# Performance work log

Hardware: AMD Instinct MI355X
Metric: run time of the kernel (lower is better)

## Reference

```python
import jax, jax.numpy as jnp
import numpy as np


def reverse_padded(tokens, lengths):
    # reverse each row within its valid length; padding stays in place
    B, T = tokens.shape
    t = jnp.arange(T)[None, :]
    L = lengths[:, None]
    idx = jnp.where(t < L, L - 1 - t, t)
    return jnp.take_along_axis(tokens, idx, axis=1)


def lstm_layer(x, lengths, Wih, Whh, bih, bhh):
    # x: [T, B, I]; emulates packed LSTM: padded steps output zeros, state frozen
    T, B, _ = x.shape
    H = Whh.shape[1]
    xW = jnp.einsum('tbi,gi->tbg', x, Wih) + bih  # precompute input GEMM [T,B,4H]
    mask = (jnp.arange(T)[:, None] < lengths[None, :]).astype(x.dtype)[:, :, None]

    def step(carry, inp):
        h, c = carry
        xw, m = inp
        gates = xw + h @ Whh.T + bhh
        i, f, g, o = jnp.split(gates, 4, axis=-1)
        i = jax.nn.sigmoid(i); f = jax.nn.sigmoid(f)
        g = jnp.tanh(g); o = jax.nn.sigmoid(o)
        c_new = f * c + i * g
        h_new = o * jnp.tanh(c_new)
        h = m * h_new + (1.0 - m) * h
        c = m * c_new + (1.0 - m) * c
        return (h, c), m * h_new

    h0 = jnp.zeros((B, H), x.dtype)
    (hT, cT), out = jax.lax.scan(step, (h0, h0), (xW, mask))
    return out


def setup_inputs() -> dict:
    key = jax.random.key(0)
    ntoken, ninp, nhid, B, T = 50000, 512, 1024, 64, 512
    ks = jax.random.split(key, 40)
    inp = {}
    inp['input'] = jax.random.randint(ks[0], (B, T), 0, ntoken)
    lens = jnp.sort(jax.random.randint(ks[1], (B,), T // 4, T + 1))[::-1]
    inp['seq_lengths'] = lens.at[0].set(T)
    inp['enc'] = jax.random.uniform(ks[2], (ntoken, ninp), jnp.float32, -0.1, 0.1)
    k = 3
    for d in ('f', 'r'):
        for l in range(2):
            I = ninp if l == 0 else nhid
            s = 1.0 / np.sqrt(nhid)
            inp[f'Wih_{d}{l}'] = jax.random.uniform(ks[k], (4 * nhid, I), jnp.float32, -s, s); k += 1
            inp[f'Whh_{d}{l}'] = jax.random.uniform(ks[k], (4 * nhid, nhid), jnp.float32, -s, s); k += 1
            inp[f'bih_{d}{l}'] = jax.random.uniform(ks[k], (4 * nhid,), jnp.float32, -s, s); k += 1
            inp[f'bhh_{d}{l}'] = jax.random.uniform(ks[k], (4 * nhid,), jnp.float32, -s, s); k += 1
    return inp


def reference(input, seq_lengths, enc,
              Wih_f0, Whh_f0, bih_f0, bhh_f0,
              Wih_f1, Whh_f1, bih_f1, bhh_f1,
              Wih_r0, Whh_r0, bih_r0, bhh_r0,
              Wih_r1, Whh_r1, bih_r1, bhh_r1):
    # eval-mode Elmo forward (all dropouts identity)
    input_rev = reverse_padded(input, seq_lengths)
    emb = enc[input].transpose(1, 0, 2)          # [T,B,ninp]
    emb_rev = enc[input_rev].transpose(1, 0, 2)  # [T,B,ninp]
    h_f = lstm_layer(emb, seq_lengths, Wih_f0, Whh_f0, bih_f0, bhh_f0)
    h_f = lstm_layer(h_f, seq_lengths, Wih_f1, Whh_f1, bih_f1, bhh_f1)
    h_r = lstm_layer(emb_rev, seq_lengths, Wih_r0, Whh_r0, bih_r0, bhh_r0)
    h_r = lstm_layer(h_r, seq_lengths, Wih_r1, Whh_r1, bih_r1, bhh_r1)
    return jnp.concatenate([h_f, h_r], axis=-1)  # [T,B,2*nhid]
```

## Files before the change

### kernel.cpp

```cpp
#include <hip/hip_runtime.h>

#define TT 512
#define BB 64
#define NI 512
#define NH 1024
#define NG 4096

using bf16x8 = __attribute__((ext_vector_type(8))) __bf16;
using f32x4  = __attribute__((ext_vector_type(4))) float;

static __device__ __forceinline__ unsigned short f2bf(float f) {
  unsigned int u = __float_as_uint(f);
  u += 0x7fffu + ((u >> 16) & 1u);
  return (unsigned short)(u >> 16);
}

__global__ void prep_layer(const float* __restrict__ Wih, const float* __restrict__ Whh,
                           const float* __restrict__ bih, const float* __restrict__ bhh,
                           unsigned short* __restrict__ Wx, unsigned short* __restrict__ Wh,
                           float* __restrict__ bias, int Kx) {
  long nx = (long)NG * Kx;
  long nh = (long)NG * NH;
  long total = nx + nh + NG;
  for (long i = (long)blockIdx.x * blockDim.x + threadIdx.x; i < total;
       i += (long)gridDim.x * blockDim.x) {
    if (i < nx) {
      int p = (int)(i / Kx); int k = (int)(i - (long)p * Kx);
      int orig = (p & 3) * NH + (p >> 2);
      Wx[i] = f2bf(Wih[(long)orig * Kx + k]);
    } else if (i < nx + nh) {
      long j = i - nx;
      int p = (int)(j / NH); int k = (int)(j - (long)p * NH);
      int orig = (p & 3) * NH + (p >> 2);
      Wh[j] = f2bf(Whh[(long)orig * NH + k]);
    } else {
      int p = (int)(i - nx - nh);
      int orig = (p & 3) * NH + (p >> 2);
      bias[p] = bih[orig] + bhh[orig];
    }
  }
}

__global__ void prep_emb(const int* __restrict__ tok, const int* __restrict__ lens,
                         const float* __restrict__ enc,
                         unsigned short* __restrict__ embf, unsigned short* __restrict__ embr) {
  int row = blockIdx.x;
  int t = row / BB, b = row - (row / BB) * BB;
  int L = lens[b];
  int tf = tok[b * TT + t];
  int ir = (t < L) ? (L - 1 - t) : t;
  int tr_ = tok[b * TT + ir];
  int i = threadIdx.x;
  float4 vf = *(const float4*)(enc + (long)tf * NI + i * 4);
  float4 vr = *(const float4*)(enc + (long)tr_ * NI + i * 4);
  ushort4 of = make_ushort4(f2bf(vf.x), f2bf(vf.y), f2bf(vf.z), f2bf(vf.w));
  ushort4 orr = make_ushort4(f2bf(vr.x), f2bf(vr.y), f2bf(vr.z), f2bf(vr.w));
  *(ushort4*)(embf + (long)row * NI + i * 4) = of;
  *(ushort4*)(embr + (long)row * NI + i * 4) = orr;
}

struct KP {
  const int* lens;
  const unsigned short* emb[2];
  const unsigned short* Wx[4];
  const unsigned short* Wh[4];
  const float* bias[4];
  unsigned short* hist[4];
  unsigned int* slots;
  float* out;
};

static __device__ __forceinline__ void poll16(const unsigned int* slots, int base,
                                              unsigned tgt) {
  const unsigned int* p = slots + (size_t)(base + ((threadIdx.x & 63) & 15)) * 8;
  for (;;) {
    unsigned v = __hip_atomic_load(p, __ATOMIC_RELAXED, __HIP_MEMORY_SCOPE_AGENT);
    if (__all((int)(v >= tgt))) break;
  }
  asm volatile("" ::: "memory");
}

template <int KQ>
static __device__ __forceinline__ void loadw_q(bf16x8* w, const unsigned short* Wsrc,
                                               int row0, int kbase, int Kfull,
                                               int ln, int kg) {
#pragma unroll
  for (int mt = 0; mt < 4; ++mt) {
    const unsigned short* p = Wsrc + (long)(row0 + mt * 16 + ln) * Kfull + kbase + kg * 8;
#pragma unroll
    for (int ks = 0; ks < KQ; ++ks) w[mt * KQ + ks] = *(const bf16x8*)(p + ks * 32);
  }
}

template <int KQ>
static __device__ __forceinline__ void gemm_row(const bf16x8* w, f32x4* acc,
                                                const unsigned short* src, int stride,
                                                int kbase, int ln, int kg) {
  const unsigned short* p0 = src + (long)ln * stride + kbase + kg * 8;
  const long rs = (long)stride * 16;
  bf16x8 b[KQ][4];
#pragma unroll
  for (int g = 0; g < KQ; ++g)
#pragma unroll
    for (int nt = 0; nt < 4; ++nt) b[g][nt] = *(const bf16x8*)(p0 + nt * rs + g * 32);
  __builtin_amdgcn_s_setprio(1);
#pragma unroll
  for (int ks = 0; ks < KQ; ++ks)
#pragma unroll
    for (int mt = 0; mt < 4; ++mt)
#pragma unroll
      for (int nt = 0; nt < 4; ++nt)
        acc[mt * 4 + nt] = __builtin_amdgcn_mfma_f32_16x16x32_bf16(
            w[mt * KQ + ks], b[ks][nt], acc[mt * 4 + nt], 0, 0, 0);
  __builtin_amdgcn_s_setprio(0);
}

template <int KQ>
static __device__ __forceinline__ void gemm_blk(const bf16x8* w, f32x4* acc,
                                                const unsigned short* src, int kbase,
                                                int ln, int kg) {
  const unsigned short* p0 = src + ((kbase >> 4) + (kg >> 1)) * 1024 + ln * 16 + (kg & 1) * 8;
  bf16x8 b[4][4];
#pragma unroll
  for (int g = 0; g < 4; ++g)
#pragma unroll
    for (int nt = 0; nt < 4; ++nt) b[g][nt] = *(const bf16x8*)(p0 + nt * 256 + g * 2048);
#pragma unroll
  for (int ks = 0; ks < KQ; ++ks) {
    __builtin_amdgcn_s_setprio(1);
#pragma unroll
    for (int mt = 0; mt < 4; ++mt)
#pragma unroll
      for (int nt = 0; nt < 4; ++nt)
        acc[mt * 4 + nt] = __builtin_amdgcn_mfma_f32_16x16x32_bf16(
            w[mt * KQ + ks], b[ks & 3][nt], acc[mt * 4 + nt], 0, 0, 0);
    __builtin_amdgcn_s_setprio(0);
    if (ks + 4 < KQ) {
#pragma unroll
      for (int nt = 0; nt < 4; ++nt)
        b[ks & 3][nt] = *(const bf16x8*)(p0 + nt * 256 + (ks + 4) * 2048);
    }
  }
}

__global__ void __launch_bounds__(512, 2) lstm_main(KP P) {
  __shared__ f32x4 red[8 * 16 * 64];
  __shared__ unsigned short hrep[64][16];
  __shared__ float hrep2[64][17];
  const int tid = threadIdx.x, lane = tid & 63, wave = tid >> 6;
  const int part = wave >> 2, q = wave & 3;
  const int wg = blockIdx.x, g = wg >> 6, wl = wg & 63;
  const int dir = g >> 1, layer = g & 1;
  const int ln = lane & 15, kg = lane >> 4;

  bf16x8 w[32];
  const int row0 = wl * 64;
  if (part == 0) {
    if (layer) loadw_q<8>(w, P.Wx[g], row0, q * 256, NH, ln, kg);
    else {
      loadw_q<4>(w, P.Wx[g], row0, q * 128, NI, ln, kg);
#pragma unroll
      for (int i = 16; i < 32; ++i) w[i] = (bf16x8)0;
    }
  } else {
    loadw_q<8>(w, P.Wh[g], row0, q * 256, NH, ln, kg);
  }
#pragma unroll
  for (int i = 0; i < 32; ++i)
    asm volatile("" : "+v"(reinterpret_cast<f32x4&>(w[i])));

  unsigned short* hist = P.hist[g];
  const unsigned short* xblk = layer ? (const unsigned short*)P.hist[g - 1] : nullptr;
  const unsigned short* xemb = P.emb[dir];

  const int i0 = wave * 2;
  const int coll = (i0 >> 2) * 4 + kg;
  const int b0 = (i0 & 3) * 16 + ln;
  const int b1 = ((i0 + 1) & 3) * 16 + ln;
  const f32x4 bias_v = *(const f32x4*)(P.bias[g] + (wl * 16 + coll) * 4);
  const int L0 = P.lens[b0], L1 = P.lens[b1];
  float c0 = 0.f, c1 = 0.f;

  const int sr = wave * 8 + (lane >> 3);
  const int sc = lane & 7;

  for (int t = 0; t < TT; ++t) {
    f32x4 acc[16];
#pragma unroll
    for (int i = 0; i < 16; ++i) { f32x4 z = {0.f, 0.f, 0.f, 0.f}; acc[i] = z; }

    if (part == 0) {
      if (layer) {
        poll16(P.slots, (g - 1) * 64 + q * 16, (unsigned)(t + 1));
        gemm_blk<8>(w, acc, xblk + (size_t)t * 65536, q * 256, ln, kg);
      } else {
        gemm_row<4>(w, acc, xemb + (long)t * BB * NI, NI, q * 128, ln, kg);
      }
    } else if (t > 0) {
      poll16(P.slots, g * 64 + q * 16, (unsigned)t);
      gemm_blk<8>(w, acc, hist + (size_t)(t - 1) * 65536, q * 256, ln, kg);
    }

#pragma unroll
    for (int i = 0; i < 16; ++i) red[(wave * 16 + i) * 64 + lane] = acc[i];
    __syncthreads();

#pragma unroll
    for (int u = 0; u < 2; ++u) {
      const int i = i0 + u;
      f32x4 gs = bias_v;
#pragma unroll
      for (int w2 = 0; w2 < 8; ++w2) gs += red[(w2 * 16 + i) * 64 + lane];
      float iv = 1.f / (1.f + __expf(-gs[0]));
      float fv = 1.f / (1.f + __expf(-gs[1]));
      float gv = 1.f - 2.f / (1.f + __expf(2.f * gs[2]));
      float og = 1.f / (1.f + __expf(-gs[3]));
      float cp = u ? c1 : c0;
      float cn = fv * cp + iv * gv;
      if (u) c1 = cn; else c0 = cn;
      float tc = 1.f - 2.f / (1.f + __expf(2.f * cn));
      float hn = og * tc;
      const int Lx = u ? L1 : L0;
      const int bx = u ? b1 : b0;
      float outv = (t < Lx) ? hn : 0.f;
      hrep[bx][coll] = f2bf(outv);
      if (layer) hrep2[bx][coll] = outv;
    }
    __syncthreads();

    {
      unsigned v = ((const unsigned*)hrep)[tid];
      __hip_atomic_store(
          (unsigned*)(hist + (size_t)t * 65536 + (size_t)wl * 1024) + tid,
          v, __ATOMIC_RELAXED, __HIP_MEMORY_SCOPE_AGENT);
    }
    asm volatile("s_waitcnt vmcnt(0)" ::: "memory");
    __syncthreads();
    if (tid == 0)
      __hip_atomic_store(P.slots + (size_t)wg * 8, (unsigned)(t + 1),
                         __ATOMIC_RELAXED, __HIP_MEMORY_SCOPE_AGENT);
    if (layer) {
#pragma unroll
      for (int u = 0; u < 2; ++u) {
        float v = hrep2[sr][sc + u * 8];
        __builtin_nontemporal_store(
            v, &P.out[(long)(t * BB + sr) * 2048 + dir * NH + wl * 16 + sc + u * 8]);
      }
    }
  }
}

extern "C" void kernel_launch(void* const* d_in, const int* in_sizes, int n_in,
                              void* d_out, int out_size, void* d_ws, size_t ws_size,
                              hipStream_t stream) {
  (void)in_sizes; (void)n_in; (void)out_size; (void)ws_size;
  const int* input = (const int*)d_in[0];
  const int* lens  = (const int*)d_in[1];
  const float* enc = (const float*)d_in[2];
  const float* Wih[4] = {(const float*)d_in[3],  (const float*)d_in[7],
                         (const float*)d_in[11], (const float*)d_in[15]};
  const float* Whh[4] = {(const float*)d_in[4],  (const float*)d_in[8],
                         (const float*)d_in[12], (const float*)d_in[16]};
  const float* bih[4] = {(const float*)d_in[5],  (const float*)d_in[9],
                         (const float*)d_in[13], (const float*)d_in[17]};
  const float* bhh[4] = {(const float*)d_in[6],  (const float*)d_in[10],
                         (const float*)d_in[14], (const float*)d_in[18]};

  char* ws = (char*)d_ws;
  size_t off = 0;
  auto carve = [&](size_t bytes) -> char* {
    char* p = ws + off;
    off += (bytes + 255) & ~(size_t)255;
    return p;
  };
  unsigned short* emb[2];
  emb[0] = (unsigned short*)carve((size_t)TT * BB * NI * 2);
  emb[1] = (unsigned short*)carve((size_t)TT * BB * NI * 2);
  unsigned short* hist[4];
  for (int g = 0; g < 4; ++g)
    hist[g] = (unsigned short*)carve((size_t)TT * BB * NH * 2);
  unsigned short* Wx[4]; unsigned short* Wh[4]; float* bias[4];
  for (int li = 0; li < 4; ++li) {
    int Kx = (li & 1) ? NH : NI;
    Wx[li]   = (unsigned short*)carve((size_t)NG * Kx * 2);
    Wh[li]   = (unsigned short*)carve((size_t)NG * NH * 2);
    bias[li] = (float*)carve((size_t)NG * 4);
  }
  unsigned int* slots = (unsigned int*)carve(256 * 32);

  hipMemsetAsync(slots, 0, 256 * 32, stream);
  for (int li = 0; li < 4; ++li) {
    int Kx = (li & 1) ? NH : NI;
    prep_layer<<<2048, 256, 0, stream>>>(Wih[li], Whh[li], bih[li], bhh[li],
                                         Wx[li], Wh[li], bias[li], Kx);
  }
  prep_emb<<<TT * BB, 128, 0, stream>>>(input, lens, enc, emb[0], emb[1]);

  KP p;
  p.lens = lens;
  p.emb[0] = emb[0]; p.emb[1] = emb[1];
  for (int li = 0; li < 4; ++li) {
    p.Wx[li] = Wx[li]; p.Wh[li] = Wh[li]; p.bias[li] = bias[li]; p.hist[li] = hist[li];
  }
  p.slots = slots;
  p.out = (float*)d_out;

  void* args[] = {&p};
  hipLaunchCooperativeKernel(lstm_main, dim3(256), dim3(512), args, 0, stream);
}
```

Before: 4.248 ms.

## Split K across all eight waves and stage recurrent h through LDS via async loads

```diff
diff --git a/kernel.cpp b/kernel.cpp
--- a/kernel.cpp
+++ b/kernel.cpp
@@ -8,6 +8,9 @@
 
 using bf16x8 = __attribute__((ext_vector_type(8))) __bf16;
 using f32x4  = __attribute__((ext_vector_type(4))) float;
+
+typedef __attribute__((address_space(3))) char       lds_char;
+typedef const __attribute__((address_space(1))) char glb_char;
 
 static __device__ __forceinline__ unsigned short f2bf(float f) {
   unsigned int u = __float_as_uint(f);
@@ -70,77 +73,21 @@
   float* out;
 };
 
-static __device__ __forceinline__ void poll16(const unsigned int* slots, int base,
-                                              unsigned tgt) {
-  const unsigned int* p = slots + (size_t)(base + ((threadIdx.x & 63) & 15)) * 8;
+static __device__ __forceinline__ void poll_comb(const unsigned int* slots, int g,
+                                                 int v, int layer, int t) {
+  const int lane = threadIdx.x & 63;
+  const bool nown = (t > 0) && (lane < 8);
+  const bool nprev = layer && (lane >= 8) && (lane < 16);
+  const unsigned int* p = slots;
+  unsigned tgt = 0u;
+  if (nown)  { p = slots + (size_t)(g * 64 + v * 8 + lane) * 8;            tgt = (unsigned)t; }
+  if (nprev) { p = slots + (size_t)((g - 1) * 64 + v * 8 + (lane - 8)) * 8; tgt = (unsigned)(t + 1); }
   for (;;) {
-    unsigned v = __hip_atomic_load(p, __ATOMIC_RELAXED, __HIP_MEMORY_SCOPE_AGENT);
-    if (__all((int)(v >= tgt))) break;
+    unsigned val = __hip_atomic_load(p, __ATOMIC_RELAXED, __HIP_MEMORY_SCOPE_AGENT);
+    if (__all((int)(val >= tgt))) break;
+    __builtin_amdgcn_s_sleep(1);
   }
   asm volatile("" ::: "memory");
-}
-
-template <int KQ>
-static __device__ __forceinline__ void loadw_q(bf16x8* w, const unsigned short* Wsrc,
-                                               int row0, int kbase, int Kfull,
-                                               int ln, int kg) {
-#pragma unroll
-  for (int mt = 0; mt < 4; ++mt) {
-    const unsigned short* p = Wsrc + (long)(row0 + mt * 16 + ln) * Kfull + kbase + kg * 8;
-#pragma unroll
-    for (int ks = 0; ks < KQ; ++ks) w[mt * KQ + ks] = *(const bf16x8*)(p + ks * 32);
-  }
-}
-
-template <int KQ>
-static __device__ __forceinline__ void gemm_row(const bf16x8* w, f32x4* acc,
-                                                const unsigned short* src, int stride,
-                                                int kbase, int ln, int kg) {
-  const unsigned short* p0 = src + (long)ln * stride + kbase + kg * 8;
-  const long rs = (long)stride * 16;
-  bf16x8 b[KQ][4];
-#pragma unroll
-  for (int g = 0; g < KQ; ++g)
-#pragma unroll
-    for (int nt = 0; nt < 4; ++nt) b[g][nt] = *(const bf16x8*)(p0 + nt * rs + g * 32);
-  __builtin_amdgcn_s_setprio(1);
-#pragma unroll
-  for (int ks = 0; ks < KQ; ++ks)
-#pragma unroll
-    for (int mt = 0; mt < 4; ++mt)
-#pragma unroll
-      for (int nt = 0; nt < 4; ++nt)
-        acc[mt * 4 + nt] = __builtin_amdgcn_mfma_f32_16x16x32_bf16(
-            w[mt * KQ + ks], b[ks][nt], acc[mt * 4 + nt], 0, 0, 0);
-  __builtin_amdgcn_s_setprio(0);
-}
-
-template <int KQ>
-static __device__ __forceinline__ void gemm_blk(const bf16x8* w, f32x4* acc,
-                                                const unsigned short* src, int kbase,
-                                                int ln, int kg) {
-  const unsigned short* p0 = src + ((kbase >> 4) + (kg >> 1)) * 1024 + ln * 16 + (kg & 1) * 8;
-  bf16x8 b[4][4];
-#pragma unroll
-  for (int g = 0; g < 4; ++g)
-#pragma unroll
-    for (int nt = 0; nt < 4; ++nt) b[g][nt] = *(const bf16x8*)(p0 + nt * 256 + g * 2048);
-#pragma unroll
-  for (int ks = 0; ks < KQ; ++ks) {
-    __builtin_amdgcn_s_setprio(1);
-#pragma unroll
-    for (int mt = 0; mt < 4; ++mt)
-#pragma unroll
-      for (int nt = 0; nt < 4; ++nt)
-        acc[mt * 4 + nt] = __builtin_amdgcn_mfma_f32_16x16x32_bf16(
-            w[mt * KQ + ks], b[ks & 3][nt], acc[mt * 4 + nt], 0, 0, 0);
-    __builtin_amdgcn_s_setprio(0);
-    if (ks + 4 < KQ) {
-#pragma unroll
-      for (int nt = 0; nt < 4; ++nt)
-        b[ks & 3][nt] = *(const bf16x8*)(p0 + nt * 256 + (ks + 4) * 2048);
-    }
-  }
 }
 
 __global__ void __launch_bounds__(512, 2) lstm_main(KP P) {
@@ -148,29 +95,48 @@
   __shared__ unsigned short hrep[64][16];
   __shared__ float hrep2[64][17];
   const int tid = threadIdx.x, lane = tid & 63, wave = tid >> 6;
-  const int part = wave >> 2, q = wave & 3;
+  const int v = wave;
   const int wg = blockIdx.x, g = wg >> 6, wl = wg & 63;
   const int dir = g >> 1, layer = g & 1;
   const int ln = lane & 15, kg = lane >> 4;
 
-  bf16x8 w[32];
+  bf16x8 wh[16], wx[16];
   const int row0 = wl * 64;
-  if (part == 0) {
-    if (layer) loadw_q<8>(w, P.Wx[g], row0, q * 256, NH, ln, kg);
-    else {
-      loadw_q<4>(w, P.Wx[g], row0, q * 128, NI, ln, kg);
-#pragma unroll
-      for (int i = 16; i < 32; ++i) w[i] = (bf16x8)0;
-    }
-  } else {
-    loadw_q<8>(w, P.Wh[g], row0, q * 256, NH, ln, kg);
-  }
-#pragma unroll
-  for (int i = 0; i < 32; ++i)
-    asm volatile("" : "+v"(reinterpret_cast<f32x4&>(w[i])));
+  {
+    const unsigned short* Wh = P.Wh[g];
+#pragma unroll
+    for (int mt = 0; mt < 4; ++mt) {
+      const unsigned short* p = Wh + (long)(row0 + mt * 16 + ln) * NH + v * 128 + kg * 8;
+#pragma unroll
+      for (int kk = 0; kk < 4; ++kk) wh[mt * 4 + kk] = *(const bf16x8*)(p + kk * 32);
+    }
+    const unsigned short* Wxp = P.Wx[g];
+    if (layer) {
+#pragma unroll
+      for (int mt = 0; mt < 4; ++mt) {
+        const unsigned short* p = Wxp + (long)(row0 + mt * 16 + ln) * NH + v * 128 + kg * 8;
+#pragma unroll
+        for (int kk = 0; kk < 4; ++kk) wx[mt * 4 + kk] = *(const bf16x8*)(p + kk * 32);
+      }
+    } else {
+#pragma unroll
+      for (int mt = 0; mt < 4; ++mt) {
+        const unsigned short* p = Wxp + (long)(row0 + mt * 16 + ln) * NI + v * 64 + kg * 8;
+#pragma unroll
+        for (int kk = 0; kk < 2; ++kk) wx[mt * 2 + kk] = *(const bf16x8*)(p + kk * 32);
+      }
+#pragma unroll
+      for (int i = 8; i < 16; ++i) wx[i] = (bf16x8)0;
+    }
+  }
+#pragma unroll
+  for (int i = 0; i < 16; ++i) {
+    asm volatile("" : "+v"(reinterpret_cast<f32x4&>(wh[i])));
+    asm volatile("" : "+v"(reinterpret_cast<f32x4&>(wx[i])));
+  }
 
   unsigned short* hist = P.hist[g];
-  const unsigned short* xblk = layer ? (const unsigned short*)P.hist[g - 1] : nullptr;
+  const unsigned short* xprev = layer ? (const unsigned short*)P.hist[g - 1] : nullptr;
   const unsigned short* xemb = P.emb[dir];
 
   const int i0 = wave * 2;
@@ -184,21 +150,85 @@
   const int sr = wave * 8 + (lane >> 3);
   const int sc = lane & 7;
 
+  lds_char* lslice = (lds_char*)((char*)red + v * 16384);
+
   for (int t = 0; t < TT; ++t) {
     f32x4 acc[16];
 #pragma unroll
     for (int i = 0; i < 16; ++i) { f32x4 z = {0.f, 0.f, 0.f, 0.f}; acc[i] = z; }
 
-    if (part == 0) {
-      if (layer) {
-        poll16(P.slots, (g - 1) * 64 + q * 16, (unsigned)(t + 1));
-        gemm_blk<8>(w, acc, xblk + (size_t)t * 65536, q * 256, ln, kg);
-      } else {
-        gemm_row<4>(w, acc, xemb + (long)t * BB * NI, NI, q * 128, ln, kg);
-      }
-    } else if (t > 0) {
-      poll16(P.slots, g * 64 + q * 16, (unsigned)t);
-      gemm_blk<8>(w, acc, hist + (size_t)(t - 1) * 65536, q * 256, ln, kg);
+    if (t > 0 || layer) poll_comb(P.slots, g, v, layer, t);
+
+    if (t > 0) {
+      const char* gsrc = (const char*)(hist + (size_t)(t - 1) * 65536 + (size_t)v * 8192);
+#pragma unroll
+      for (int c = 0; c < 16; ++c) {
+        __builtin_amdgcn_global_load_lds(
+            (glb_char*)(gsrc + c * 1024 + lane * 16),
+            (lds_char*)(lslice + c * 1024), 16, 0, 0);
+      }
+    }
+
+    if (layer) {
+      const unsigned short* pb = xprev + (size_t)t * 65536 +
+          (size_t)(v * 8 + (kg >> 1)) * 1024 + ln * 16 + (kg & 1) * 8;
+      bf16x8 bx[4][4];
+#pragma unroll
+      for (int kk = 0; kk < 4; ++kk)
+#pragma unroll
+        for (int nt = 0; nt < 4; ++nt)
+          bx[kk][nt] = *(const bf16x8*)(pb + kk * 2048 + nt * 256);
+#pragma unroll
+      for (int kk = 0; kk < 4; ++kk)
+#pragma unroll
+        for (int mt = 0; mt < 4; ++mt)
+#pragma unroll
+          for (int nt = 0; nt < 4; ++nt)
+            acc[mt * 4 + nt] = __builtin_amdgcn_mfma_f32_16x16x32_bf16(
+                wx[mt * 4 + kk], bx[kk][nt], acc[mt * 4 + nt], 0, 0, 0);
+    } else {
+      const unsigned short* pb = xemb + ((size_t)t * BB + ln) * NI + v * 64 + kg * 8;
+      bf16x8 bx[2][4];
+#pragma unroll
+      for (int kk = 0; kk < 2; ++kk)
+#pragma unroll
+        for (int nt = 0; nt < 4; ++nt)
+          bx[kk][nt] = *(const bf16x8*)(pb + kk * 32 + (size_t)nt * 16 * NI);
+#pragma unroll
+      for (int kk = 0; kk < 2; ++kk)
+#pragma unroll
+        for (int mt = 0; mt < 4; ++mt)
+#pragma unroll
+          for (int nt = 0; nt < 4; ++nt)
+            acc[mt * 4 + nt] = __builtin_amdgcn_mfma_f32_16x16x32_bf16(
+                wx[mt * 2 + kk], bx[kk][nt], acc[mt * 4 + nt], 0, 0, 0);
+    }
+
+    if (t > 0) {
+      asm volatile("s_waitcnt vmcnt(0)" ::: "memory");
+      __builtin_amdgcn_sched_barrier(0);
+      const char* ls = (const char*)red + v * 16384 +
+                       (kg >> 1) * 2048 + ln * 32 + (kg & 1) * 16;
+      bf16x8 bh[2][4];
+#pragma unroll
+      for (int nt = 0; nt < 4; ++nt)
+        bh[0][nt] = *(const bf16x8*)(ls + nt * 512);
+#pragma unroll
+      for (int kk = 0; kk < 4; ++kk) {
+        if (kk < 3) {
+#pragma unroll
+          for (int nt = 0; nt < 4; ++nt)
+            bh[(kk + 1) & 1][nt] = *(const bf16x8*)(ls + (kk + 1) * 4096 + nt * 512);
+        }
+#pragma unroll
+        for (int mt = 0; mt < 4; ++mt)
+#pragma unroll
+          for (int nt = 0; nt < 4; ++nt)
+            acc[mt * 4 + nt] = __builtin_amdgcn_mfma_f32_16x16x32_bf16(
+                wh[mt * 4 + kk], bh[kk & 1][nt], acc[mt * 4 + nt], 0, 0, 0);
+      }
+      asm volatile("s_waitcnt lgkmcnt(0)" ::: "memory");
+      __builtin_amdgcn_sched_barrier(0);
     }
 
 #pragma unroll
@@ -229,10 +259,10 @@
     __syncthreads();
 
     {
-      unsigned v = ((const unsigned*)hrep)[tid];
+      unsigned vv = ((const unsigned*)hrep)[tid];
       __hip_atomic_store(
           (unsigned*)(hist + (size_t)t * 65536 + (size_t)wl * 1024) + tid,
-          v, __ATOMIC_RELAXED, __HIP_MEMORY_SCOPE_AGENT);
+          vv, __ATOMIC_RELAXED, __HIP_MEMORY_SCOPE_AGENT);
     }
     asm volatile("s_waitcnt vmcnt(0)" ::: "memory");
     __syncthreads();
@@ -242,9 +272,9 @@
     if (layer) {
 #pragma unroll
       for (int u = 0; u < 2; ++u) {
-        float v = hrep2[sr][sc + u * 8];
+        float vv = hrep2[sr][sc + u * 8];
         __builtin_nontemporal_store(
-            v, &P.out[(long)(t * BB + sr) * 2048 + dir * NH + wl * 16 + sc + u * 8]);
+            vv, &P.out[(long)(t * BB + sr) * 2048 + dir * NH + wl * 16 + sc + u * 8]);
       }
     }
   }
```

Result: faster. 3.934 ms (-7.4%).
